# Kernel tuning notes

Measured on AMD Instinct MI355X. Metric: run time of the kernel, lower is better.

## Reference

```python
import jax, jax.numpy as jnp
import numpy as np

EMBED_DIM = 1024
NUM_HEADS = 16
HEAD_DIM = EMBED_DIM // NUM_HEADS
BATCH = 2
SEQ = 2048


def setup_inputs() -> dict:
    key = jax.random.key(0)
    ks = jax.random.split(key, 10)
    s = 1.0 / np.sqrt(EMBED_DIM)
    inp = {
        "query": jax.random.normal(ks[0], (BATCH, SEQ, EMBED_DIM), jnp.float32),
        # Linear weights stored as [in, out] (y = x @ W + b)
        "wq": jax.random.normal(ks[1], (EMBED_DIM, EMBED_DIM), jnp.float32) * s,
        "bq": jnp.zeros((EMBED_DIM,), jnp.float32),
        "wk": jax.random.normal(ks[2], (EMBED_DIM, EMBED_DIM), jnp.float32) * s,
        "bk": jnp.zeros((EMBED_DIM,), jnp.float32),
        "wv": jax.random.normal(ks[3], (EMBED_DIM, EMBED_DIM), jnp.float32) * s,
        "bv": jnp.zeros((EMBED_DIM,), jnp.float32),
        "wo": jax.random.normal(ks[4], (EMBED_DIM, EMBED_DIM), jnp.float32) * s,
        "bo": jnp.zeros((EMBED_DIM,), jnp.float32),
        "temperature": jnp.float32(HEAD_DIM),  # learnable temperature, init = head_dim
    }
    return inp


def reference(query, wq, bq, wk, bk, wv, bv, wo, bo, temperature):
    B, S, E = query.shape
    # self-attention: key = value = query
    Q = (query @ wq + bq).reshape(B, S, NUM_HEADS, HEAD_DIM).transpose(0, 2, 1, 3)
    K = (query @ wk + bk).reshape(B, S, NUM_HEADS, HEAD_DIM).transpose(0, 2, 1, 3)
    V = (query @ wv + bv).reshape(B, S, NUM_HEADS, HEAD_DIM).transpose(0, 2, 1, 3)
    # squared Euclidean distances: ||q||^2 + ||k||^2 - 2<q,k>
    q_sq = jnp.sum(Q * Q, axis=-1, keepdims=True)          # (B,H,Sq,1)
    k_sq = jnp.sum(K * K, axis=-1, keepdims=True)          # (B,H,Sk,1)
    qk = jnp.einsum("bhqd,bhkd->bhqk", Q, K)
    d_sq = jnp.maximum(q_sq + jnp.swapaxes(k_sq, -2, -1) - 2.0 * qk, 0.0)
    attn = jax.nn.softmax(-d_sq / temperature, axis=-1)    # (B,H,Sq,Sk)
    out = jnp.einsum("bhqk,bhkd->bhqd", attn, V)
    out = out.transpose(0, 2, 1, 3).reshape(B, S, E)
    return out @ wo + bo
```

## Files before the change

kernel.cpp:

```cpp
#include <hip/hip_runtime.h>
#include <stdint.h>
#include <stddef.h>


#define LOG2E 1.44269504088896f

typedef __attribute__((ext_vector_type(8))) short bf16x8;
typedef __attribute__((ext_vector_type(4))) float f32x4;
typedef __attribute__((ext_vector_type(4))) unsigned short u16x4;
typedef __attribute__((ext_vector_type(8))) unsigned short u16x8;

__device__ __forceinline__ unsigned short f2b(float f) {
  union { float f; unsigned int u; } x; x.f = f;
  unsigned int u = x.u;
  u += 0x7fffu + ((u >> 16) & 1u);
  return (unsigned short)(u >> 16);
}
__device__ __forceinline__ float b2f(unsigned short s) {
  union { unsigned int u; float f; } x; x.u = ((unsigned int)s) << 16;
  return x.f;
}

#define GLD_LDS(g, l) __builtin_amdgcn_global_load_lds( \
    (const __attribute__((address_space(1))) void*)(g), \
    (__attribute__((address_space(3))) void*)(l), 16, 0, 0)

__global__ void convx_kernel(const float* __restrict__ X, unsigned short* __restrict__ Xb) {
  int i = (blockIdx.x * 256 + threadIdx.x) * 4;
  f32x4 v = *(const f32x4*)&X[i];
  u16x4 o;
  #pragma unroll
  for (int j = 0; j < 4; ++j) o[j] = f2b(v[j]);
  *(u16x4*)&Xb[i] = o;
}

__global__ void transw_kernel(const float* __restrict__ wq, const float* __restrict__ wk,
                              const float* __restrict__ wv, const float* __restrict__ wo,
                              unsigned short* __restrict__ WTqkv, unsigned short* __restrict__ WTo) {
  __shared__ float tile[64][65];
  int z = blockIdx.z;
  const float* src = (z == 0) ? wq : (z == 1) ? wk : (z == 2) ? wv : wo;
  unsigned short* dst = (z < 3) ? (WTqkv + (size_t)z * 1024 * 1024) : WTo;
  int k0 = blockIdx.y * 64, n0 = blockIdx.x * 64;
  int rr = threadIdx.x >> 6, cc = threadIdx.x & 63;
  #pragma unroll
  for (int p = 0; p < 16; ++p) {
    int row = p * 4 + rr;
    tile[row][cc] = src[(size_t)(k0 + row) * 1024 + n0 + cc];
  }
  __syncthreads();
  #pragma unroll
  for (int p = 0; p < 16; ++p) {
    int row = p * 4 + rr;
    dst[(size_t)(n0 + row) * 1024 + k0 + cc] = f2b(tile[cc][row]);
  }
}

__global__ __launch_bounds__(256, 2) void gemm_qkv_kernel(
    const unsigned short* __restrict__ X, const unsigned short* __restrict__ WT,
    const float* __restrict__ bq, const float* __restrict__ bk, const float* __restrict__ bv,
    unsigned short* __restrict__ Qb, unsigned short* __restrict__ Kb,
    unsigned short* __restrict__ VTo) {
  __shared__ unsigned short As[128 * 32];
  __shared__ unsigned short Bs[128 * 32];
  const int t = threadIdx.x, w = t >> 6, lane = t & 63;
  const int r = lane & 15, q4 = lane >> 4;
  const int m0 = blockIdx.y * 128, n0 = blockIdx.x * 128;
  const int wr = (w >> 1) * 64, wc = (w & 1) * 64;
  const unsigned short* Xg = X + (size_t)m0 * 1024;
  const unsigned short* Wg = WT + (size_t)n0 * 1024;
  f32x4 acc[4][4] = {};
  for (int k0 = 0; k0 < 1024; k0 += 32) {
    #pragma unroll
    for (int g = 0; g < 2; ++g) {
      int slot = g * 256 + t;
      int row = slot >> 2, ko = (slot & 3) * 8;
      GLD_LDS(Xg + (size_t)row * 1024 + k0 + ko, &As[(g * 256 + w * 64) * 8]);
      GLD_LDS(Wg + (size_t)row * 1024 + k0 + ko, &Bs[(g * 256 + w * 64) * 8]);
    }
    __syncthreads();
    bf16x8 af[4], bfr[4];
    #pragma unroll
    for (int mf = 0; mf < 4; ++mf)
      af[mf] = *(const bf16x8*)&As[(wr + mf * 16 + r) * 32 + q4 * 8];
    #pragma unroll
    for (int nf = 0; nf < 4; ++nf)
      bfr[nf] = *(const bf16x8*)&Bs[(wc + nf * 16 + r) * 32 + q4 * 8];
    #pragma unroll
    for (int mf = 0; mf < 4; ++mf)
      #pragma unroll
      for (int nf = 0; nf < 4; ++nf)
        acc[mf][nf] = __builtin_amdgcn_mfma_f32_16x16x32_bf16(af[mf], bfr[nf], acc[mf][nf], 0, 0, 0);
    __syncthreads();
  }
  const int nblk = n0 >> 10;
  if (nblk < 2) {
    const float* bias = (nblk == 0) ? bq : bk;
    unsigned short* OutB = (nblk == 0) ? Qb : Kb;
    const int nc0 = n0 & 1023;
    #pragma unroll
    for (int nf = 0; nf < 4; ++nf) {
      int n = nc0 + wc + nf * 16 + r;
      float bb = bias[n];
      #pragma unroll
      for (int mf = 0; mf < 4; ++mf) {
        int m = m0 + wr + mf * 16 + q4 * 4;
        f32x4 v = acc[mf][nf];
        #pragma unroll
        for (int i = 0; i < 4; ++i)
          OutB[(size_t)(m + i) * 1024 + n] = f2b(v[i] + bb);
      }
    }
  } else {
    const int c0 = n0 - 2048;
    #pragma unroll
    for (int nf = 0; nf < 4; ++nf) {
      int c = c0 + wc + nf * 16 + r;
      float bb = bv[c];
      int h = c >> 6, d = c & 63;
      #pragma unroll
      for (int mf = 0; mf < 4; ++mf) {
        int m = m0 + wr + mf * 16 + q4 * 4;
        int b = m >> 11, s = m & 2047;
        f32x4 v = acc[mf][nf];
        u16x4 pk;
        #pragma unroll
        for (int i = 0; i < 4; ++i) pk[i] = f2b(v[i] + bb);
        *(u16x4*)&VTo[((size_t)((b * 16 + h) * 64 + d)) * 2048 + s] = pk;
      }
    }
  }
}

__global__ void sumsq_kernel(const unsigned short* __restrict__ Qb,
                             const unsigned short* __restrict__ Kb,
                             const float* __restrict__ temp,
                             float* __restrict__ qs2, float* __restrict__ ks2) {
  int idx = blockIdx.x * 256 + threadIdx.x;
  int bh = idx >> 11, s = idx & 2047;
  int b = bh >> 4, h = bh & 15;
  const u16x8* qp = (const u16x8*)(Qb + (size_t)(b * 2048 + s) * 1024 + h * 64);
  const u16x8* kp = (const u16x8*)(Kb + (size_t)(b * 2048 + s) * 1024 + h * 64);
  float scale = LOG2E / temp[0];
  float sq = 0.f, sk = 0.f;
  #pragma unroll
  for (int c = 0; c < 8; ++c) {
    u16x8 vq = qp[c], vk = kp[c];
    #pragma unroll
    for (int j = 0; j < 8; ++j) {
      float q = b2f(vq[j]); sq += q * q;
      float k = b2f(vk[j]); sk += k * k;
    }
  }
  qs2[idx] = sq * scale;
  ks2[idx] = sk * scale;
}

__global__ __launch_bounds__(256, 2) void flash_kernel(
    const unsigned short* __restrict__ Qb, const unsigned short* __restrict__ Kb,
    const unsigned short* __restrict__ VT, const float* __restrict__ qs2,
    const float* __restrict__ ks2, const float* __restrict__ temp,
    unsigned short* __restrict__ AO) {
  __shared__ unsigned short Ks[2 * 128 * 32];
  __shared__ unsigned short Vs[4 * 64 * 32];
  __shared__ unsigned short Ps[4][32 * 68];
  const int t = threadIdx.x, w = t >> 6, lane = t & 63;
  const int r = lane & 15, q4 = lane >> 4;
  const int bh = blockIdx.y, b = bh >> 4, h = bh & 15;
  const int q0 = blockIdx.x * 128;
  const float cc = 2.0f * LOG2E / temp[0];

  bf16x8 qf[2][2];
  #pragma unroll
  for (int mf = 0; mf < 2; ++mf) {
    int sq = q0 + w * 32 + mf * 16 + r;
    const unsigned short* qp = Qb + (size_t)(b * 2048 + sq) * 1024 + h * 64;
    #pragma unroll
    for (int ks = 0; ks < 2; ++ks) qf[mf][ks] = *(const bf16x8*)(qp + ks * 32 + q4 * 8);
  }
  f32x4 qsv[2];
  #pragma unroll
  for (int mf = 0; mf < 2; ++mf)
    qsv[mf] = *(const f32x4*)&qs2[bh * 2048 + q0 + w * 32 + mf * 16 + q4 * 4];

  f32x4 accO[2][4] = {};
  f32x4 lsum[2] = {};
  bf16x8 ones;
  #pragma unroll
  for (int j = 0; j < 8; ++j) ones[j] = (short)0x3F80;

  for (int key0 = 0; key0 < 2048; key0 += 128) {
    #pragma unroll
    for (int g = 0; g < 4; ++g) {
      int slot = g * 256 + t;
      int half = slot >> 9, key = (slot >> 2) & 127, ko = (slot & 3) * 8;
      GLD_LDS(Kb + (size_t)(b * 2048 + key0 + key) * 1024 + h * 64 + half * 32 + ko,
              &Ks[(g * 256 + w * 64) * 8]);
      int kh = slot >> 8, dd = (slot >> 2) & 63, kk = (slot & 3) * 8;
      GLD_LDS(VT + (size_t)(bh * 64 + dd) * 2048 + key0 + kh * 32 + kk,
              &Vs[(g * 256 + w * 64) * 8]);
    }
    float ksv[8];
    #pragma unroll
    for (int j = 0; j < 8; ++j) ksv[j] = ks2[bh * 2048 + key0 + j * 16 + r];
    __syncthreads();

    #pragma unroll
    for (int hh = 0; hh < 2; ++hh) {
      f32x4 accS[2][4] = {};
      #pragma unroll
      for (int ks = 0; ks < 2; ++ks) {
        #pragma unroll
        for (int nf = 0; nf < 4; ++nf) {
          bf16x8 kf = *(const bf16x8*)&Ks[(ks * 128 + hh * 64 + nf * 16 + r) * 32 + q4 * 8];
          accS[0][nf] = __builtin_amdgcn_mfma_f32_16x16x32_bf16(qf[0][ks], kf, accS[0][nf], 0, 0, 0);
          accS[1][nf] = __builtin_amdgcn_mfma_f32_16x16x32_bf16(qf[1][ks], kf, accS[1][nf], 0, 0, 0);
        }
      }
      #pragma unroll
      for (int mf = 0; mf < 2; ++mf) {
        #pragma unroll
        for (int nf = 0; nf < 4; ++nf) {
          float kq = ksv[hh * 4 + nf];
          #pragma unroll
          for (int i = 0; i < 4; ++i) {
            float u = cc * accS[mf][nf][i] - kq - qsv[mf][i];
            float p = __builtin_amdgcn_exp2f(fminf(u, 0.f));
            Ps[w][(mf * 16 + q4 * 4 + i) * 68 + nf * 16 + r] = f2b(p);
          }
        }
      }
      #pragma unroll
      for (int ks = 0; ks < 2; ++ks) {
        bf16x8 vb[4];
        #pragma unroll
        for (int df = 0; df < 4; ++df)
          vb[df] = *(const bf16x8*)&Vs[((hh * 2 + ks) * 64 + df * 16 + r) * 32 + q4 * 8];
        #pragma unroll
        for (int mf = 0; mf < 2; ++mf) {
          bf16x8 pa = *(const bf16x8*)&Ps[w][(mf * 16 + r) * 68 + ks * 32 + q4 * 8];
          lsum[mf] = __builtin_amdgcn_mfma_f32_16x16x32_bf16(pa, ones, lsum[mf], 0, 0, 0);
          #pragma unroll
          for (int df = 0; df < 4; ++df)
            accO[mf][df] = __builtin_amdgcn_mfma_f32_16x16x32_bf16(pa, vb[df], accO[mf][df], 0, 0, 0);
        }
      }
    }
    __syncthreads();
  }
  #pragma unroll
  for (int mf = 0; mf < 2; ++mf) {
    float inv[4];
    #pragma unroll
    for (int i = 0; i < 4; ++i) inv[i] = 1.0f / lsum[mf][i];
    #pragma unroll
    for (int df = 0; df < 4; ++df) {
      int d = df * 16 + r;
      #pragma unroll
      for (int i = 0; i < 4; ++i) {
        int sq = q0 + w * 32 + mf * 16 + q4 * 4 + i;
        AO[(size_t)(b * 2048 + sq) * 1024 + h * 64 + d] = f2b(accO[mf][df][i] * inv[i]);
      }
    }
  }
}

__global__ __launch_bounds__(256, 2) void gemm_out_kernel(
    const unsigned short* __restrict__ A, const unsigned short* __restrict__ WT,
    const float* __restrict__ bo, float* __restrict__ Out) {
  __shared__ unsigned short As[128 * 32];
  __shared__ unsigned short Bs[128 * 32];
  const int t = threadIdx.x, w = t >> 6, lane = t & 63;
  const int r = lane & 15, q4 = lane >> 4;
  const int m0 = blockIdx.y * 128, n0 = blockIdx.x * 128;
  const int wr = (w >> 1) * 64, wc = (w & 1) * 64;
  const unsigned short* Ag = A + (size_t)m0 * 1024;
  const unsigned short* Wg = WT + (size_t)n0 * 1024;
  f32x4 acc[4][4] = {};
  for (int k0 = 0; k0 < 1024; k0 += 32) {
    #pragma unroll
    for (int g = 0; g < 2; ++g) {
      int slot = g * 256 + t;
      int row = slot >> 2, ko = (slot & 3) * 8;
      GLD_LDS(Ag + (size_t)row * 1024 + k0 + ko, &As[(g * 256 + w * 64) * 8]);
      GLD_LDS(Wg + (size_t)row * 1024 + k0 + ko, &Bs[(g * 256 + w * 64) * 8]);
    }
    __syncthreads();
    bf16x8 af[4], bfr[4];
    #pragma unroll
    for (int mf = 0; mf < 4; ++mf)
      af[mf] = *(const bf16x8*)&As[(wr + mf * 16 + r) * 32 + q4 * 8];
    #pragma unroll
    for (int nf = 0; nf < 4; ++nf)
      bfr[nf] = *(const bf16x8*)&Bs[(wc + nf * 16 + r) * 32 + q4 * 8];
    #pragma unroll
    for (int mf = 0; mf < 4; ++mf)
      #pragma unroll
      for (int nf = 0; nf < 4; ++nf)
        acc[mf][nf] = __builtin_amdgcn_mfma_f32_16x16x32_bf16(af[mf], bfr[nf], acc[mf][nf], 0, 0, 0);
    __syncthreads();
  }
  #pragma unroll
  for (int nf = 0; nf < 4; ++nf) {
    int n = n0 + wc + nf * 16 + r;
    float bb = bo[n];
    #pragma unroll
    for (int mf = 0; mf < 4; ++mf) {
      int m = m0 + wr + mf * 16 + q4 * 4;
      f32x4 v = acc[mf][nf];
      #pragma unroll
      for (int i = 0; i < 4; ++i)
        Out[(size_t)(m + i) * 1024 + n] = v[i] + bb;
    }
  }
}

extern "C" void kernel_launch(void* const* d_in, const int* in_sizes, int n_in,
                              void* d_out, int out_size, void* d_ws, size_t ws_size,
                              hipStream_t stream) {
  const float* X    = (const float*)d_in[0];
  const float* wq   = (const float*)d_in[1];
  const float* bq   = (const float*)d_in[2];
  const float* wk   = (const float*)d_in[3];
  const float* bk   = (const float*)d_in[4];
  const float* wv   = (const float*)d_in[5];
  const float* bv   = (const float*)d_in[6];
  const float* wo   = (const float*)d_in[7];
  const float* bo   = (const float*)d_in[8];
  const float* temp = (const float*)d_in[9];
  float* Out = (float*)d_out;

  char* ws = (char*)d_ws;
  unsigned short* Xb    = (unsigned short*)ws; ws += (size_t)4096 * 1024 * 2;
  unsigned short* WTqkv = (unsigned short*)ws; ws += (size_t)3072 * 1024 * 2;
  unsigned short* WTo   = (unsigned short*)ws; ws += (size_t)1024 * 1024 * 2;
  unsigned short* Qb    = (unsigned short*)ws; ws += (size_t)4096 * 1024 * 2;
  unsigned short* Kb    = (unsigned short*)ws; ws += (size_t)4096 * 1024 * 2;
  unsigned short* VT    = (unsigned short*)ws; ws += (size_t)4096 * 1024 * 2;
  unsigned short* AO    = (unsigned short*)ws; ws += (size_t)4096 * 1024 * 2;
  float* qs2 = (float*)ws; ws += (size_t)65536 * 4;
  float* ks2 = (float*)ws; ws += (size_t)65536 * 4;

  convx_kernel<<<4096, 256, 0, stream>>>(X, Xb);
  transw_kernel<<<dim3(16, 16, 4), 256, 0, stream>>>(wq, wk, wv, wo, WTqkv, WTo);
  gemm_qkv_kernel<<<dim3(24, 32), 256, 0, stream>>>(Xb, WTqkv, bq, bk, bv, Qb, Kb, VT);
  sumsq_kernel<<<256, 256, 0, stream>>>(Qb, Kb, temp, qs2, ks2);
  flash_kernel<<<dim3(16, 32), 256, 0, stream>>>(Qb, Kb, VT, qs2, ks2, temp, AO);
  gemm_out_kernel<<<dim3(8, 32), 256, 0, stream>>>(AO, WTo, bo, Out);
}
```

Measured before the change: 222.1 us.

## Double-buffer flash K/V tiles, widen GEMM K-steps, shrink out-proj tile

The flash kernel now walks keys in 64-key chunks and keeps two LDS buffers, so the next K/V chunk and its key norms are fetched while the current chunk is computed. This needs only one barrier per chunk. The QKV and output GEMMs load 64-wide K slices per barrier pair, halving the number of syncs. The output GEMM uses 128x64 tiles so it launches twice as many blocks and fills more CUs. P is now converted to bf16 by truncation instead of rounding, which adds a small precision bias.

```diff
diff --git a/kernel.cpp b/kernel.cpp
--- a/kernel.cpp
+++ b/kernel.cpp
@@ -61,8 +61,8 @@
     const float* __restrict__ bq, const float* __restrict__ bk, const float* __restrict__ bv,
     unsigned short* __restrict__ Qb, unsigned short* __restrict__ Kb,
     unsigned short* __restrict__ VTo) {
-  __shared__ unsigned short As[128 * 32];
-  __shared__ unsigned short Bs[128 * 32];
+  __shared__ unsigned short As[2 * 128 * 32];
+  __shared__ unsigned short Bs[2 * 128 * 32];
   const int t = threadIdx.x, w = t >> 6, lane = t & 63;
   const int r = lane & 15, q4 = lane >> 4;
   const int m0 = blockIdx.y * 128, n0 = blockIdx.x * 128;
@@ -70,27 +70,30 @@
   const unsigned short* Xg = X + (size_t)m0 * 1024;
   const unsigned short* Wg = WT + (size_t)n0 * 1024;
   f32x4 acc[4][4] = {};
-  for (int k0 = 0; k0 < 1024; k0 += 32) {
-    #pragma unroll
-    for (int g = 0; g < 2; ++g) {
+  for (int k0 = 0; k0 < 1024; k0 += 64) {
+    #pragma unroll
+    for (int g = 0; g < 4; ++g) {
       int slot = g * 256 + t;
-      int row = slot >> 2, ko = (slot & 3) * 8;
-      GLD_LDS(Xg + (size_t)row * 1024 + k0 + ko, &As[(g * 256 + w * 64) * 8]);
-      GLD_LDS(Wg + (size_t)row * 1024 + k0 + ko, &Bs[(g * 256 + w * 64) * 8]);
-    }
-    __syncthreads();
-    bf16x8 af[4], bfr[4];
-    #pragma unroll
-    for (int mf = 0; mf < 4; ++mf)
-      af[mf] = *(const bf16x8*)&As[(wr + mf * 16 + r) * 32 + q4 * 8];
-    #pragma unroll
-    for (int nf = 0; nf < 4; ++nf)
-      bfr[nf] = *(const bf16x8*)&Bs[(wc + nf * 16 + r) * 32 + q4 * 8];
-    #pragma unroll
-    for (int mf = 0; mf < 4; ++mf)
+      int kh = slot >> 9, row = (slot >> 2) & 127, ko = (slot & 3) * 8;
+      GLD_LDS(Xg + (size_t)row * 1024 + k0 + kh * 32 + ko, &As[(g * 256 + w * 64) * 8]);
+      GLD_LDS(Wg + (size_t)row * 1024 + k0 + kh * 32 + ko, &Bs[(g * 256 + w * 64) * 8]);
+    }
+    __syncthreads();
+    #pragma unroll
+    for (int kh = 0; kh < 2; ++kh) {
+      bf16x8 af[4], bfr[4];
+      #pragma unroll
+      for (int mf = 0; mf < 4; ++mf)
+        af[mf] = *(const bf16x8*)&As[kh * 4096 + (wr + mf * 16 + r) * 32 + q4 * 8];
       #pragma unroll
       for (int nf = 0; nf < 4; ++nf)
-        acc[mf][nf] = __builtin_amdgcn_mfma_f32_16x16x32_bf16(af[mf], bfr[nf], acc[mf][nf], 0, 0, 0);
+        bfr[nf] = *(const bf16x8*)&Bs[kh * 4096 + (wc + nf * 16 + r) * 32 + q4 * 8];
+      #pragma unroll
+      for (int mf = 0; mf < 4; ++mf)
+        #pragma unroll
+        for (int nf = 0; nf < 4; ++nf)
+          acc[mf][nf] = __builtin_amdgcn_mfma_f32_16x16x32_bf16(af[mf], bfr[nf], acc[mf][nf], 0, 0, 0);
+    }
     __syncthreads();
   }
   const int nblk = n0 >> 10;
@@ -161,8 +164,8 @@
     const unsigned short* __restrict__ VT, const float* __restrict__ qs2,
     const float* __restrict__ ks2, const float* __restrict__ temp,
     unsigned short* __restrict__ AO) {
-  __shared__ unsigned short Ks[2 * 128 * 32];
-  __shared__ unsigned short Vs[4 * 64 * 32];
+  __shared__ unsigned short Ks[2][2 * 64 * 32];
+  __shared__ unsigned short Vs[2][2 * 64 * 32];
   __shared__ unsigned short Ps[4][32 * 68];
   const int t = threadIdx.x, w = t >> 6, lane = t & 63;
   const int r = lane & 15, q4 = lane >> 4;
@@ -189,64 +192,82 @@
   #pragma unroll
   for (int j = 0; j < 8; ++j) ones[j] = (short)0x3F80;
 
-  for (int key0 = 0; key0 < 2048; key0 += 128) {
-    #pragma unroll
-    for (int g = 0; g < 4; ++g) {
-      int slot = g * 256 + t;
-      int half = slot >> 9, key = (slot >> 2) & 127, ko = (slot & 3) * 8;
-      GLD_LDS(Kb + (size_t)(b * 2048 + key0 + key) * 1024 + h * 64 + half * 32 + ko,
-              &Ks[(g * 256 + w * 64) * 8]);
-      int kh = slot >> 8, dd = (slot >> 2) & 63, kk = (slot & 3) * 8;
-      GLD_LDS(VT + (size_t)(bh * 64 + dd) * 2048 + key0 + kh * 32 + kk,
-              &Vs[(g * 256 + w * 64) * 8]);
-    }
-    float ksv[8];
-    #pragma unroll
-    for (int j = 0; j < 8; ++j) ksv[j] = ks2[bh * 2048 + key0 + j * 16 + r];
-    __syncthreads();
-
-    #pragma unroll
-    for (int hh = 0; hh < 2; ++hh) {
-      f32x4 accS[2][4] = {};
-      #pragma unroll
-      for (int ks = 0; ks < 2; ++ks) {
-        #pragma unroll
-        for (int nf = 0; nf < 4; ++nf) {
-          bf16x8 kf = *(const bf16x8*)&Ks[(ks * 128 + hh * 64 + nf * 16 + r) * 32 + q4 * 8];
-          accS[0][nf] = __builtin_amdgcn_mfma_f32_16x16x32_bf16(qf[0][ks], kf, accS[0][nf], 0, 0, 0);
-          accS[1][nf] = __builtin_amdgcn_mfma_f32_16x16x32_bf16(qf[1][ks], kf, accS[1][nf], 0, 0, 0);
+  const unsigned short* Kg = Kb + ((size_t)b * 2048) * 1024 + h * 64;
+  const unsigned short* Vg = VT + ((size_t)bh * 64) * 2048;
+  const float* kqb = ks2 + bh * 2048 + r;
+
+  #pragma unroll
+  for (int g = 0; g < 2; ++g) {
+    int slot = g * 256 + t;
+    int half = slot >> 8, key = (slot >> 2) & 63, ko = (slot & 3) * 8;
+    GLD_LDS(Kg + (size_t)key * 1024 + half * 32 + ko, &Ks[0][(g * 256 + w * 64) * 8]);
+    GLD_LDS(Vg + (size_t)key * 2048 + half * 32 + ko, &Vs[0][(g * 256 + w * 64) * 8]);
+  }
+  float kq[4];
+  #pragma unroll
+  for (int nf = 0; nf < 4; ++nf) kq[nf] = kqb[nf * 16];
+
+  #pragma unroll 2
+  for (int c = 0; c < 32; ++c) {
+    const int buf = c & 1;
+    __syncthreads();
+    float kqn[4];
+    if (c < 31) {
+      #pragma unroll
+      for (int g = 0; g < 2; ++g) {
+        int slot = g * 256 + t;
+        int half = slot >> 8, key = (slot >> 2) & 63, ko = (slot & 3) * 8;
+        GLD_LDS(Kg + (size_t)((c + 1) * 64 + key) * 1024 + half * 32 + ko,
+                &Ks[buf ^ 1][(g * 256 + w * 64) * 8]);
+        GLD_LDS(Vg + (size_t)key * 2048 + (c + 1) * 64 + half * 32 + ko,
+                &Vs[buf ^ 1][(g * 256 + w * 64) * 8]);
+      }
+      #pragma unroll
+      for (int nf = 0; nf < 4; ++nf) kqn[nf] = kqb[(c + 1) * 64 + nf * 16];
+    }
+
+    f32x4 accS[2][4] = {};
+    #pragma unroll
+    for (int ks = 0; ks < 2; ++ks) {
+      #pragma unroll
+      for (int nf = 0; nf < 4; ++nf) {
+        bf16x8 kf = *(const bf16x8*)&Ks[buf][(ks * 64 + nf * 16 + r) * 32 + q4 * 8];
+        accS[0][nf] = __builtin_amdgcn_mfma_f32_16x16x32_bf16(qf[0][ks], kf, accS[0][nf], 0, 0, 0);
+        accS[1][nf] = __builtin_amdgcn_mfma_f32_16x16x32_bf16(qf[1][ks], kf, accS[1][nf], 0, 0, 0);
+      }
+    }
+    #pragma unroll
+    for (int mf = 0; mf < 2; ++mf) {
+      #pragma unroll
+      for (int nf = 0; nf < 4; ++nf) {
+        #pragma unroll
+        for (int i = 0; i < 4; ++i) {
+          float u = __builtin_fmaf(cc, accS[mf][nf][i], -kq[nf] - qsv[mf][i]);
+          float p = __builtin_amdgcn_exp2f(fminf(u, 0.f));
+          union { float f; unsigned int u; } pu; pu.f = p;
+          Ps[w][(mf * 16 + q4 * 4 + i) * 68 + nf * 16 + r] = (unsigned short)(pu.u >> 16);
         }
       }
+    }
+    #pragma unroll
+    for (int ks = 0; ks < 2; ++ks) {
+      bf16x8 vb[4];
+      #pragma unroll
+      for (int df = 0; df < 4; ++df)
+        vb[df] = *(const bf16x8*)&Vs[buf][(ks * 64 + df * 16 + r) * 32 + q4 * 8];
       #pragma unroll
       for (int mf = 0; mf < 2; ++mf) {
-        #pragma unroll
-        for (int nf = 0; nf < 4; ++nf) {
-          float kq = ksv[hh * 4 + nf];
-          #pragma unroll
-          for (int i = 0; i < 4; ++i) {
-            float u = cc * accS[mf][nf][i] - kq - qsv[mf][i];
-            float p = __builtin_amdgcn_exp2f(fminf(u, 0.f));
-            Ps[w][(mf * 16 + q4 * 4 + i) * 68 + nf * 16 + r] = f2b(p);
-          }
-        }
-      }
-      #pragma unroll
-      for (int ks = 0; ks < 2; ++ks) {
-        bf16x8 vb[4];
+        bf16x8 pa = *(const bf16x8*)&Ps[w][(mf * 16 + r) * 68 + ks * 32 + q4 * 8];
+        lsum[mf] = __builtin_amdgcn_mfma_f32_16x16x32_bf16(pa, ones, lsum[mf], 0, 0, 0);
         #pragma unroll
         for (int df = 0; df < 4; ++df)
-          vb[df] = *(const bf16x8*)&Vs[((hh * 2 + ks) * 64 + df * 16 + r) * 32 + q4 * 8];
-        #pragma unroll
-        for (int mf = 0; mf < 2; ++mf) {
-          bf16x8 pa = *(const bf16x8*)&Ps[w][(mf * 16 + r) * 68 + ks * 32 + q4 * 8];
-          lsum[mf] = __builtin_amdgcn_mfma_f32_16x16x32_bf16(pa, ones, lsum[mf], 0, 0, 0);
-          #pragma unroll
-          for (int df = 0; df < 4; ++df)
-            accO[mf][df] = __builtin_amdgcn_mfma_f32_16x16x32_bf16(pa, vb[df], accO[mf][df], 0, 0, 0);
-        }
-      }
-    }
-    __syncthreads();
+          accO[mf][df] = __builtin_amdgcn_mfma_f32_16x16x32_bf16(pa, vb[df], accO[mf][df], 0, 0, 0);
+      }
+    }
+    if (c < 31) {
+      #pragma unroll
+      for (int nf = 0; nf < 4; ++nf) kq[nf] = kqn[nf];
+    }
   }
   #pragma unroll
   for (int mf = 0; mf < 2; ++mf) {
@@ -268,40 +289,48 @@
 __global__ __launch_bounds__(256, 2) void gemm_out_kernel(
     const unsigned short* __restrict__ A, const unsigned short* __restrict__ WT,
     const float* __restrict__ bo, float* __restrict__ Out) {
-  __shared__ unsigned short As[128 * 32];
-  __shared__ unsigned short Bs[128 * 32];
+  __shared__ unsigned short As[2 * 128 * 32];
+  __shared__ unsigned short Bs[2 * 64 * 32];
   const int t = threadIdx.x, w = t >> 6, lane = t & 63;
   const int r = lane & 15, q4 = lane >> 4;
-  const int m0 = blockIdx.y * 128, n0 = blockIdx.x * 128;
-  const int wr = (w >> 1) * 64, wc = (w & 1) * 64;
+  const int m0 = blockIdx.y * 128, n0 = blockIdx.x * 64;
+  const int wr = (w >> 1) * 64, wc = (w & 1) * 32;
   const unsigned short* Ag = A + (size_t)m0 * 1024;
   const unsigned short* Wg = WT + (size_t)n0 * 1024;
-  f32x4 acc[4][4] = {};
-  for (int k0 = 0; k0 < 1024; k0 += 32) {
+  f32x4 acc[4][2] = {};
+  for (int k0 = 0; k0 < 1024; k0 += 64) {
+    #pragma unroll
+    for (int g = 0; g < 4; ++g) {
+      int slot = g * 256 + t;
+      int kh = slot >> 9, row = (slot >> 2) & 127, ko = (slot & 3) * 8;
+      GLD_LDS(Ag + (size_t)row * 1024 + k0 + kh * 32 + ko, &As[(g * 256 + w * 64) * 8]);
+    }
     #pragma unroll
     for (int g = 0; g < 2; ++g) {
       int slot = g * 256 + t;
-      int row = slot >> 2, ko = (slot & 3) * 8;
-      GLD_LDS(Ag + (size_t)row * 1024 + k0 + ko, &As[(g * 256 + w * 64) * 8]);
-      GLD_LDS(Wg + (size_t)row * 1024 + k0 + ko, &Bs[(g * 256 + w * 64) * 8]);
-    }
-    __syncthreads();
-    bf16x8 af[4], bfr[4];
-    #pragma unroll
-    for (int mf = 0; mf < 4; ++mf)
-      af[mf] = *(const bf16x8*)&As[(wr + mf * 16 + r) * 32 + q4 * 8];
-    #pragma unroll
-    for (int nf = 0; nf < 4; ++nf)
-      bfr[nf] = *(const bf16x8*)&Bs[(wc + nf * 16 + r) * 32 + q4 * 8];
-    #pragma unroll
-    for (int mf = 0; mf < 4; ++mf)
-      #pragma unroll
-      for (int nf = 0; nf < 4; ++nf)
-        acc[mf][nf] = __builtin_amdgcn_mfma_f32_16x16x32_bf16(af[mf], bfr[nf], acc[mf][nf], 0, 0, 0);
-    __syncthreads();
-  }
-  #pragma unroll
-  for (int nf = 0; nf < 4; ++nf) {
+      int kh = slot >> 8, row = (slot >> 2) & 63, ko = (slot & 3) * 8;
+      GLD_LDS(Wg + (size_t)row * 1024 + k0 + kh * 32 + ko, &Bs[(g * 256 + w * 64) * 8]);
+    }
+    __syncthreads();
+    #pragma unroll
+    for (int kh = 0; kh < 2; ++kh) {
+      bf16x8 af[4], bfr[2];
+      #pragma unroll
+      for (int mf = 0; mf < 4; ++mf)
+        af[mf] = *(const bf16x8*)&As[kh * 4096 + (wr + mf * 16 + r) * 32 + q4 * 8];
+      #pragma unroll
+      for (int nf = 0; nf < 2; ++nf)
+        bfr[nf] = *(const bf16x8*)&Bs[kh * 2048 + (wc + nf * 16 + r) * 32 + q4 * 8];
+      #pragma unroll
+      for (int mf = 0; mf < 4; ++mf)
+        #pragma unroll
+        for (int nf = 0; nf < 2; ++nf)
+          acc[mf][nf] = __builtin_amdgcn_mfma_f32_16x16x32_bf16(af[mf], bfr[nf], acc[mf][nf], 0, 0, 0);
+    }
+    __syncthreads();
+  }
+  #pragma unroll
+  for (int nf = 0; nf < 2; ++nf) {
     int n = n0 + wc + nf * 16 + r;
     float bb = bo[n];
     #pragma unroll
@@ -346,5 +375,5 @@
   gemm_qkv_kernel<<<dim3(24, 32), 256, 0, stream>>>(Xb, WTqkv, bq, bk, bv, Qb, Kb, VT);
   sumsq_kernel<<<256, 256, 0, stream>>>(Qb, Kb, temp, qs2, ks2);
   flash_kernel<<<dim3(16, 32), 256, 0, stream>>>(Qb, Kb, VT, qs2, ks2, temp, AO);
-  gemm_out_kernel<<<dim3(8, 32), 256, 0, stream>>>(AO, WTo, bo, Out);
-}
+  gemm_out_kernel<<<dim3(16, 32), 256, 0, stream>>>(AO, WTo, bo, Out);
+}
```

Result: faster. 209.8 us (-5.5%).
